# Optimization experiments

Hardware: AMD Instinct MI355X
Metric: run time of the kernel (lower is better)

Reference implementation:

```python
import jax, jax.numpy as jnp
import numpy as np


def setup_inputs() -> dict:
    key = jax.random.key(0)
    k1, k2, k3, k4 = jax.random.split(key, 4)
    N, M, D = 4096, 4096, 1024
    H = jax.random.normal(k1, (N, D), dtype=jnp.float32)
    K = jax.random.normal(k2, (M, D), dtype=jnp.float32)
    V = jax.random.normal(k3, (M, D), dtype=jnp.float32)
    attn_mask = jax.random.uniform(k4, (N, M), dtype=jnp.float32)
    return {"H": H, "K": K, "V": V, "attn_mask": attn_mask}


def reference(H, K, V, attn_mask):
    # scores: [N, M] = H @ K^T, scaled by sqrt(d)
    d = H.shape[1]
    scores = jnp.matmul(H, K.T) / jnp.sqrt(jnp.asarray(d, dtype=H.dtype))
    # double softmax with elementwise mask multiply in between
    probs = jax.nn.softmax(jax.nn.softmax(scores, axis=1) * attn_mask, axis=1)
    return jnp.matmul(probs, V)
```

## Files before the change

### kernel.cpp

```cpp
#include <hip/hip_runtime.h>
#include <cstdint>

typedef unsigned short u16;
typedef __bf16 bf16x8 __attribute__((ext_vector_type(8)));
typedef float f32x4 __attribute__((ext_vector_type(4)));
typedef unsigned int u32x4 __attribute__((ext_vector_type(4)));

__device__ __forceinline__ float bf2f(u16 h) {
  union { unsigned int u; float f; } v; v.u = ((unsigned int)h) << 16; return v.f;
}
__device__ __forceinline__ u16 f2bf(float f) {
  union { float f; unsigned int u; } v; v.f = f;
  unsigned int u = v.u;
  return (u16)((u + 0x7FFFu + ((u >> 16) & 1u)) >> 16);
}

__device__ __forceinline__ void ld_lds16(const void* g, void* l) {
  __builtin_amdgcn_global_load_lds(
      (const __attribute__((address_space(1))) unsigned int*)g,
      (__attribute__((address_space(3))) unsigned int*)l, 16, 0, 0);
}

__global__ __launch_bounds__(256) void gemm1_kernel(
    const u16* __restrict__ A, const u16* __restrict__ B,
    u16* __restrict__ S, int ldA, int ldB, int ldC)
{
  __shared__ u16 smem[128 * 64 * 2];
  u16* As = smem;
  u16* Bs = smem + 8192;
  u16* epi = smem;

  const int tid  = threadIdx.x;
  const int lane = tid & 63;
  const int w    = tid >> 6;
  const int wr   = w >> 1;
  const int wc   = w & 1;
  const int quad = lane >> 4;
  const int cIn  = lane & 15;

  const int flat = blockIdx.x;
  const int xcd  = flat & 7;
  const int i    = flat >> 3;
  const int rowBlk = ((xcd >> 2) * 16 + (i & 15)) * 128;
  const int colBlk = ((xcd & 3) * 8 + (i >> 4)) * 128;

  const int lrow   = lane >> 3;
  const int gchunk = (lane & 7) ^ lrow;

  f32x4 acc[4][4];
  #pragma unroll
  for (int a = 0; a < 4; ++a)
    #pragma unroll
    for (int b = 0; b < 4; ++b) acc[a][b] = {0.f, 0.f, 0.f, 0.f};

  for (int k0 = 0; k0 < 1024; k0 += 64) {
    #pragma unroll
    for (int t = 0; t < 4; ++t) {
      int rg = w * 4 + t;
      const u16* ga = A + (size_t)(rowBlk + rg * 8 + lrow) * ldA + k0 + gchunk * 8;
      const u16* gb = B + (size_t)(colBlk + rg * 8 + lrow) * ldB + k0 + gchunk * 8;
      ld_lds16(ga, &As[rg * 512]);
      ld_lds16(gb, &Bs[rg * 512]);
    }
    __syncthreads();

    #pragma unroll
    for (int ks = 0; ks < 2; ++ks) {
      bf16x8 af[4], bfr[4];
      #pragma unroll
      for (int mi = 0; mi < 4; ++mi) {
        int row = wr * 64 + mi * 16 + cIn;
        int ch  = (ks * 4 + quad) ^ (row & 7);
        af[mi]  = *(const bf16x8*)&As[row * 64 + ch * 8];
      }
      #pragma unroll
      for (int ni = 0; ni < 4; ++ni) {
        int row = wc * 64 + ni * 16 + cIn;
        int ch  = (ks * 4 + quad) ^ (row & 7);
        bfr[ni] = *(const bf16x8*)&Bs[row * 64 + ch * 8];
      }
      #pragma unroll
      for (int mi = 0; mi < 4; ++mi)
        #pragma unroll
        for (int ni = 0; ni < 4; ++ni)
          acc[mi][ni] = __builtin_amdgcn_mfma_f32_16x16x32_bf16(
              af[mi], bfr[ni], acc[mi][ni], 0, 0, 0);
    }
    __syncthreads();
  }

  const float scale = 0.03125f;
  #pragma unroll
  for (int mi = 0; mi < 4; ++mi) {
    #pragma unroll
    for (int ni = 0; ni < 4; ++ni) {
      int colT = wc * 64 + ni * 16 + cIn;
      #pragma unroll
      for (int r = 0; r < 4; ++r) {
        int band = wr * 16 + quad * 4 + r;
        epi[band * 136 + colT] = f2bf(acc[mi][ni][r] * scale);
      }
    }
    __syncthreads();
    #pragma unroll
    for (int it = 0; it < 2; ++it) {
      int j   = it * 256 + tid;
      int rr  = j >> 4;
      int c8  = j & 15;
      int grow = rowBlk + (rr >> 4) * 64 + mi * 16 + (rr & 15);
      u32x4 v = *(const u32x4*)&epi[rr * 136 + c8 * 8];
      *(u32x4*)&S[(size_t)grow * ldC + colBlk + c8 * 8] = v;
    }
    __syncthreads();
  }
}

__global__ __launch_bounds__(256) void gemm2_kernel(
    const u16* __restrict__ A, const u16* __restrict__ B,
    float* __restrict__ Out, const float* __restrict__ L2,
    int ldA, int ldB, int ldC)
{
  __shared__ u16 As[2 * 64 * 64];
  __shared__ u16 Bs[2 * 128 * 64];

  const int tid  = threadIdx.x;
  const int lane = tid & 63;
  const int w    = tid >> 6;
  const int wrow = w >> 1;
  const int wcol = w & 1;
  const int quad = lane >> 4;
  const int cIn  = lane & 15;

  const int flat = blockIdx.x;
  const int xcd  = flat & 7;
  const int i    = flat >> 3;
  const int rowBlk = (xcd * 8 + (i & 7)) * 64;
  const int colBlk = (i >> 3) * 128;

  const int lrow   = lane >> 3;
  const int gchunk = (lane & 7) ^ lrow;

  f32x4 acc[2][4];
  #pragma unroll
  for (int a = 0; a < 2; ++a)
    #pragma unroll
    for (int b = 0; b < 4; ++b) acc[a][b] = {0.f, 0.f, 0.f, 0.f};

  for (int k0 = 0; k0 < 4096; k0 += 128) {
    #pragma unroll
    for (int h = 0; h < 2; ++h) {
      int kk = k0 + h * 64;
      #pragma unroll
      for (int t = 0; t < 2; ++t) {
        int rg = w * 2 + t;
        const u16* ga = A + (size_t)(rowBlk + rg * 8 + lrow) * ldA + kk + gchunk * 8;
        ld_lds16(ga, &As[h * 4096 + rg * 512]);
      }
      #pragma unroll
      for (int t = 0; t < 4; ++t) {
        int rg = w * 4 + t;
        const u16* gb = B + (size_t)(colBlk + rg * 8 + lrow) * ldB + kk + gchunk * 8;
        ld_lds16(gb, &Bs[h * 8192 + rg * 512]);
      }
    }
    __syncthreads();

    #pragma unroll
    for (int h = 0; h < 2; ++h) {
      #pragma unroll
      for (int ks = 0; ks < 2; ++ks) {
        bf16x8 af[2], bfr[4];
        #pragma unroll
        for (int mi = 0; mi < 2; ++mi) {
          int row = wrow * 32 + mi * 16 + cIn;
          int ch  = (ks * 4 + quad) ^ (row & 7);
          af[mi]  = *(const bf16x8*)&As[h * 4096 + row * 64 + ch * 8];
        }
        #pragma unroll
        for (int ni = 0; ni < 4; ++ni) {
          int row = wcol * 64 + ni * 16 + cIn;
          int ch  = (ks * 4 + quad) ^ (row & 7);
          bfr[ni] = *(const bf16x8*)&Bs[h * 8192 + row * 64 + ch * 8];
        }
        #pragma unroll
        for (int mi = 0; mi < 2; ++mi)
          #pragma unroll
          for (int ni = 0; ni < 4; ++ni)
            acc[mi][ni] = __builtin_amdgcn_mfma_f32_16x16x32_bf16(
                af[mi], bfr[ni], acc[mi][ni], 0, 0, 0);
      }
    }
    __syncthreads();
  }

  #pragma unroll
  for (int mi = 0; mi < 2; ++mi) {
    #pragma unroll
    for (int r = 0; r < 4; ++r) {
      int row   = rowBlk + wrow * 32 + mi * 16 + quad * 4 + r;
      float inv = 1.0f / L2[row];
      #pragma unroll
      for (int ni = 0; ni < 4; ++ni) {
        int col = colBlk + wcol * 64 + ni * 16 + cIn;
        __builtin_nontemporal_store(acc[mi][ni][r] * inv,
                                    &Out[(size_t)row * ldC + col]);
      }
    }
  }
}

__global__ __launch_bounds__(256) void prep_kernel(
    const float* __restrict__ H, const float* __restrict__ Kin,
    const float* __restrict__ V, u16* __restrict__ Hb, u16* __restrict__ Kb,
    u16* __restrict__ Vt)
{
  int b = blockIdx.x;
  if (b < 8192) {
    const float* src = (b < 4096) ? H : Kin;
    u16* dst = (b < 4096) ? Hb : Kb;
    int i = (b & 4095) * 256 + threadIdx.x;
    float4 v = ((const float4*)src)[i];
    ushort4 o;
    o.x = f2bf(v.x); o.y = f2bf(v.y); o.z = f2bf(v.z); o.w = f2bf(v.w);
    ((ushort4*)dst)[i] = o;
  } else {
    __shared__ float tile[32][33];
    b -= 8192;
    int c0 = (b & 31) * 32;
    int r0 = (b >> 5) * 32;
    int tx = threadIdx.x & 31, ty = threadIdx.x >> 5;
    #pragma unroll
    for (int s = 0; s < 32; s += 8)
      tile[ty + s][tx] = V[(size_t)(r0 + ty + s) * 1024 + c0 + tx];
    __syncthreads();
    #pragma unroll
    for (int s = 0; s < 32; s += 8)
      Vt[(size_t)(c0 + ty + s) * 4096 + r0 + tx] = f2bf(tile[tx][ty + s]);
  }
}

__global__ __launch_bounds__(256) void softmax2_kernel(
    u16* __restrict__ S, const float* __restrict__ mask,
    float* __restrict__ L2, int M)
{
  int row = blockIdx.x;
  u16* srow = S + (size_t)row * M;
  const float* mrow = mask + (size_t)row * M;
  const int base = threadIdx.x * 16;

  u16 sl[16];
  *(uint4*)(sl)     = *(const uint4*)(srow + base);
  *(uint4*)(sl + 8) = *(const uint4*)(srow + base + 8);

  float e[16];
  float s1 = 0.f;
  #pragma unroll
  for (int j = 0; j < 16; ++j) { e[j] = __expf(bf2f(sl[j])); s1 += e[j]; }

  __shared__ float wred[8];
  #pragma unroll
  for (int m = 1; m < 64; m <<= 1) s1 += __shfl_xor(s1, m, 64);
  if ((threadIdx.x & 63) == 0) wred[threadIdx.x >> 6] = s1;
  __syncthreads();
  float inv = 1.0f / (wred[0] + wred[1] + wred[2] + wred[3]);

  float mv[16];
  #pragma unroll
  for (int q = 0; q < 4; ++q)
    *(float4*)(mv + q * 4) = *(const float4*)(mrow + base + q * 4);

  float lsum = 0.f;
  #pragma unroll
  for (int j = 0; j < 16; ++j) {
    float p = __expf(e[j] * inv * mv[j]);
    lsum += p;
    sl[j] = f2bf(p);
  }
  *(uint4*)(srow + base)     = *(uint4*)(sl);
  *(uint4*)(srow + base + 8) = *(uint4*)(sl + 8);

  #pragma unroll
  for (int m = 1; m < 64; m <<= 1) lsum += __shfl_xor(lsum, m, 64);
  if ((threadIdx.x & 63) == 0) wred[4 + (threadIdx.x >> 6)] = lsum;
  __syncthreads();
  if (threadIdx.x == 0) L2[row] = wred[4] + wred[5] + wred[6] + wred[7];
}

extern "C" void kernel_launch(void* const* d_in, const int* in_sizes, int n_in,
                              void* d_out, int out_size, void* d_ws, size_t ws_size,
                              hipStream_t stream) {
  const float* H    = (const float*)d_in[0];
  const float* Kin  = (const float*)d_in[1];
  const float* V    = (const float*)d_in[2];
  const float* mask = (const float*)d_in[3];
  float* out = (float*)d_out;

  const int N = 4096, M = 4096, D = 1024;

  char* ws = (char*)d_ws;
  u16*   Hb = (u16*)(ws);
  u16*   Kb = (u16*)(ws + (8ull << 20));
  u16*   Vt = (u16*)(ws + (16ull << 20));
  u16*   S  = (u16*)(ws + (24ull << 20));
  float* L2 = (float*)(ws + (56ull << 20));

  prep_kernel<<<dim3(12288), dim3(256), 0, stream>>>(H, Kin, V, Hb, Kb, Vt);

  gemm1_kernel<<<dim3(1024), dim3(256), 0, stream>>>(Hb, Kb, S, D, D, M);

  softmax2_kernel<<<dim3(N), dim3(256), 0, stream>>>(S, mask, L2, M);

  gemm2_kernel<<<dim3(512), dim3(256), 0, stream>>>(S, Vt, out, L2, M, M, D);
}
```

Before: 233.7 us.

## Store scores in 4-row interleaved layout, drop LDS epilogue, vectorise V transpose

The GEMM1 epilogue now writes bf16 scores straight from registers as 4-element vectors into a row-group-interleaved layout (groups of 4 rows interleaved by column). This removes the LDS staging and the barriers. The softmax kernel is rewritten to process 4 rows per block, reading that interleaved layout and writing normal row-major probabilities back for GEMM2. The V transpose in prep now handles 64x32 tiles, converts to bf16 before LDS, and issues 16-byte stores. The trade-off is narrower 8-byte scattered stores in GEMM1 and higher register use in softmax.

```diff
diff --git a/kernel.cpp b/kernel.cpp
--- a/kernel.cpp
+++ b/kernel.cpp
@@ -5,6 +5,8 @@
 typedef __bf16 bf16x8 __attribute__((ext_vector_type(8)));
 typedef float f32x4 __attribute__((ext_vector_type(4)));
 typedef unsigned int u32x4 __attribute__((ext_vector_type(4)));
+typedef unsigned short u16x4 __attribute__((ext_vector_type(4)));
+typedef unsigned short u16x8 __attribute__((ext_vector_type(8)));
 
 __device__ __forceinline__ float bf2f(u16 h) {
   union { unsigned int u; float f; } v; v.u = ((unsigned int)h) << 16; return v.f;
@@ -23,12 +25,10 @@
 
 __global__ __launch_bounds__(256) void gemm1_kernel(
     const u16* __restrict__ A, const u16* __restrict__ B,
-    u16* __restrict__ S, int ldA, int ldB, int ldC)
+    u16* __restrict__ S, int ldA, int ldB)
 {
-  __shared__ u16 smem[128 * 64 * 2];
-  u16* As = smem;
-  u16* Bs = smem + 8192;
-  u16* epi = smem;
+  __shared__ u16 As[128 * 64];
+  __shared__ u16 Bs[128 * 64];
 
   const int tid  = threadIdx.x;
   const int lane = tid & 63;
@@ -92,26 +92,15 @@
   const float scale = 0.03125f;
   #pragma unroll
   for (int mi = 0; mi < 4; ++mi) {
+    int grp = (rowBlk >> 2) + wr * 16 + mi * 4 + quad;
     #pragma unroll
     for (int ni = 0; ni < 4; ++ni) {
-      int colT = wc * 64 + ni * 16 + cIn;
-      #pragma unroll
-      for (int r = 0; r < 4; ++r) {
-        int band = wr * 16 + quad * 4 + r;
-        epi[band * 136 + colT] = f2bf(acc[mi][ni][r] * scale);
-      }
-    }
-    __syncthreads();
-    #pragma unroll
-    for (int it = 0; it < 2; ++it) {
-      int j   = it * 256 + tid;
-      int rr  = j >> 4;
-      int c8  = j & 15;
-      int grow = rowBlk + (rr >> 4) * 64 + mi * 16 + (rr & 15);
-      u32x4 v = *(const u32x4*)&epi[rr * 136 + c8 * 8];
-      *(u32x4*)&S[(size_t)grow * ldC + colBlk + c8 * 8] = v;
-    }
-    __syncthreads();
+      int col = colBlk + wc * 64 + ni * 16 + cIn;
+      u16x4 v;
+      #pragma unroll
+      for (int r = 0; r < 4; ++r) v[r] = f2bf(acc[mi][ni][r] * scale);
+      *(u16x4*)&S[((size_t)grp * 4096 + col) * 4] = v;
+    }
   }
 }
 
@@ -224,66 +213,99 @@
     o.x = f2bf(v.x); o.y = f2bf(v.y); o.z = f2bf(v.z); o.w = f2bf(v.w);
     ((ushort4*)dst)[i] = o;
   } else {
-    __shared__ float tile[32][33];
+    __shared__ u16 tile[32 * 72];
     b -= 8192;
+    int r0 = (b >> 5) * 64;
     int c0 = (b & 31) * 32;
-    int r0 = (b >> 5) * 32;
-    int tx = threadIdx.x & 31, ty = threadIdx.x >> 5;
-    #pragma unroll
-    for (int s = 0; s < 32; s += 8)
-      tile[ty + s][tx] = V[(size_t)(r0 + ty + s) * 1024 + c0 + tx];
-    __syncthreads();
-    #pragma unroll
-    for (int s = 0; s < 32; s += 8)
-      Vt[(size_t)(c0 + ty + s) * 4096 + r0 + tx] = f2bf(tile[tx][ty + s]);
+    int row = threadIdx.x >> 2;
+    int f4  = threadIdx.x & 3;
+    #pragma unroll
+    for (int j = 0; j < 2; ++j) {
+      float4 v = *(const float4*)&V[(size_t)(r0 + row) * 1024 + c0 + (f4 * 2 + j) * 4];
+      int cc = f4 * 8 + j * 4;
+      tile[(cc + 0) * 72 + row] = f2bf(v.x);
+      tile[(cc + 1) * 72 + row] = f2bf(v.y);
+      tile[(cc + 2) * 72 + row] = f2bf(v.z);
+      tile[(cc + 3) * 72 + row] = f2bf(v.w);
+    }
+    __syncthreads();
+    int cc2   = threadIdx.x >> 3;
+    int chunk = threadIdx.x & 7;
+    u16x8 o = *(const u16x8*)&tile[cc2 * 72 + chunk * 8];
+    *(u16x8*)&Vt[(size_t)(c0 + cc2) * 4096 + r0 + chunk * 8] = o;
   }
 }
 
 __global__ __launch_bounds__(256) void softmax2_kernel(
     u16* __restrict__ S, const float* __restrict__ mask,
-    float* __restrict__ L2, int M)
+    float* __restrict__ L2)
 {
-  int row = blockIdx.x;
-  u16* srow = S + (size_t)row * M;
-  const float* mrow = mask + (size_t)row * M;
-  const int base = threadIdx.x * 16;
-
-  u16 sl[16];
-  *(uint4*)(sl)     = *(const uint4*)(srow + base);
-  *(uint4*)(sl + 8) = *(const uint4*)(srow + base + 8);
-
-  float e[16];
-  float s1 = 0.f;
-  #pragma unroll
-  for (int j = 0; j < 16; ++j) { e[j] = __expf(bf2f(sl[j])); s1 += e[j]; }
-
-  __shared__ float wred[8];
-  #pragma unroll
-  for (int m = 1; m < 64; m <<= 1) s1 += __shfl_xor(s1, m, 64);
-  if ((threadIdx.x & 63) == 0) wred[threadIdx.x >> 6] = s1;
+  const int g = blockIdx.x;
+  const int t = threadIdx.x;
+  u16* chunk = S + (size_t)g * 16384;
+
+  u16 sv[64];
+  #pragma unroll
+  for (int q = 0; q < 8; ++q)
+    *(u32x4*)(sv + q * 8) = *(const u32x4*)(chunk + t * 64 + q * 8);
+  float mv[4][16];
+  #pragma unroll
+  for (int r = 0; r < 4; ++r)
+    #pragma unroll
+    for (int q = 0; q < 4; ++q)
+      *(f32x4*)(&mv[r][q * 4]) =
+          *(const f32x4*)(mask + (size_t)(g * 4 + r) * 4096 + t * 16 + q * 4);
+
+  float e[4][16];
+  float p1[4] = {0.f, 0.f, 0.f, 0.f};
+  #pragma unroll
+  for (int c = 0; c < 16; ++c)
+    #pragma unroll
+    for (int r = 0; r < 4; ++r) {
+      e[r][c] = __expf(bf2f(sv[c * 4 + r]));
+      p1[r] += e[r][c];
+    }
+
+  __shared__ float wred1[4][4], wred2[4][4];
+  #pragma unroll
+  for (int m = 1; m < 64; m <<= 1)
+    #pragma unroll
+    for (int r = 0; r < 4; ++r) p1[r] += __shfl_xor(p1[r], m, 64);
+  if ((t & 63) == 0)
+    #pragma unroll
+    for (int r = 0; r < 4; ++r) wred1[t >> 6][r] = p1[r];
   __syncthreads();
-  float inv = 1.0f / (wred[0] + wred[1] + wred[2] + wred[3]);
-
-  float mv[16];
-  #pragma unroll
-  for (int q = 0; q < 4; ++q)
-    *(float4*)(mv + q * 4) = *(const float4*)(mrow + base + q * 4);
-
-  float lsum = 0.f;
-  #pragma unroll
-  for (int j = 0; j < 16; ++j) {
-    float p = __expf(e[j] * inv * mv[j]);
-    lsum += p;
-    sl[j] = f2bf(p);
-  }
-  *(uint4*)(srow + base)     = *(uint4*)(sl);
-  *(uint4*)(srow + base + 8) = *(uint4*)(sl + 8);
-
-  #pragma unroll
-  for (int m = 1; m < 64; m <<= 1) lsum += __shfl_xor(lsum, m, 64);
-  if ((threadIdx.x & 63) == 0) wred[4 + (threadIdx.x >> 6)] = lsum;
+
+  float inv1[4];
+  #pragma unroll
+  for (int r = 0; r < 4; ++r)
+    inv1[r] = 1.0f / (wred1[0][r] + wred1[1][r] + wred1[2][r] + wred1[3][r]);
+
+  float s2[4] = {0.f, 0.f, 0.f, 0.f};
+  #pragma unroll
+  for (int r = 0; r < 4; ++r) {
+    u16 pv[16];
+    #pragma unroll
+    for (int c = 0; c < 16; ++c) {
+      float p = __expf(e[r][c] * inv1[r] * mv[r][c]);
+      s2[r] += p;
+      pv[c] = f2bf(p);
+    }
+    u16* dst = S + (size_t)(g * 4 + r) * 4096 + t * 16;
+    *(u32x4*)(dst)     = *(const u32x4*)(pv);
+    *(u32x4*)(dst + 8) = *(const u32x4*)(pv + 8);
+  }
+
+  #pragma unroll
+  for (int m = 1; m < 64; m <<= 1)
+    #pragma unroll
+    for (int r = 0; r < 4; ++r) s2[r] += __shfl_xor(s2[r], m, 64);
+  if ((t & 63) == 0)
+    #pragma unroll
+    for (int r = 0; r < 4; ++r) wred2[t >> 6][r] = s2[r];
   __syncthreads();
-  if (threadIdx.x == 0) L2[row] = wred[4] + wred[5] + wred[6] + wred[7];
+  if (t < 4)
+    L2[g * 4 + t] = wred2[0][t] + wred2[1][t] + wred2[2][t] + wred2[3][t];
 }
 
 extern "C" void kernel_launch(void* const* d_in, const int* in_sizes, int n_in,
@@ -304,11 +326,11 @@
   u16*   S  = (u16*)(ws + (24ull << 20));
   float* L2 = (float*)(ws + (56ull << 20));
 
-  prep_kernel<<<dim3(12288), dim3(256), 0, stream>>>(H, Kin, V, Hb, Kb, Vt);
-
-  gemm1_kernel<<<dim3(1024), dim3(256), 0, stream>>>(Hb, Kb, S, D, D, M);
-
-  softmax2_kernel<<<dim3(N), dim3(256), 0, stream>>>(S, mask, L2, M);
+  prep_kernel<<<dim3(10240), dim3(256), 0, stream>>>(H, Kin, V, Hb, Kb, Vt);
+
+  gemm1_kernel<<<dim3(1024), dim3(256), 0, stream>>>(Hb, Kb, S, D, D);
+
+  softmax2_kernel<<<dim3(N / 4), dim3(256), 0, stream>>>(S, mask, L2);
 
   gemm2_kernel<<<dim3(512), dim3(256), 0, stream>>>(S, Vt, out, L2, M, M, D);
 }
```

After: 238.8 us. 1.02x slower.
